# Kernel optimization log

Hardware: AMD Instinct MI355X
Metric: run time of the kernel (lower is better)

## Reference

```python
import jax, jax.numpy as jnp
import numpy as np

B, C, Q, D = 64, 2, 64, 4096
VOCAB = 30000


def setup_inputs() -> dict:
    key = jax.random.key(0)
    k1, k2, k3, k4, k5 = jax.random.split(key, 5)
    simmat = jax.random.uniform(k1, (B, C, Q, D), dtype=jnp.float32, minval=-1.0, maxval=1.0)
    dlens = jax.random.randint(k2, (B,), D // 2, D + 1, dtype=jnp.int32)
    qlens = jax.random.randint(k3, (B,), Q // 2, Q + 1, dtype=jnp.int32)
    dtoks = jax.random.randint(k4, (B, D), 0, VOCAB, dtype=jnp.int32)
    qtoks = jax.random.randint(k5, (B, Q), 0, VOCAB, dtype=jnp.int32)
    # -1 marks padding tokens beyond the true lengths
    dtoks = jnp.where(jnp.arange(D)[None, :] < dlens[:, None], dtoks, -1)
    qtoks = jnp.where(jnp.arange(Q)[None, :] < qlens[:, None], qtoks, -1)
    return {"simmat": simmat, "dlens": dlens, "dtoks": dtoks, "qtoks": qtoks, "nbins": 29}


def reference(simmat, dlens, dtoks, qtoks, nbins):
    b, c, q, d = simmat.shape
    # bin index per similarity value (int truncation, as in torch .int())
    bins = ((simmat + 1.00001) / 2.0 * (nbins - 1)).astype(jnp.int32)  # [B,C,Q,D]
    # weight = 1 where both doc token and query token are real (not padding)
    w = ((dtoks != -1)[:, None, :] & (qtoks != -1)[:, :, None]).astype(simmat.dtype)  # [B,Q,D]
    wb = jnp.broadcast_to(w[:, None, :, :], (b, c, q, d))
    # vectorized weighted histogram: scatter-add along bins per (b,c,q) row
    rows = jnp.arange(b * c * q)[:, None]
    hist = jnp.zeros((b * c * q, nbins), dtype=simmat.dtype)
    hist = hist.at[rows, bins.reshape(-1, d)].add(wb.reshape(-1, d))
    return hist.reshape(b, c, q, nbins)
```

## Files before the change

### kernel.cpp

```cpp
#include <hip/hip_runtime.h>

#define THREADS 256
#define NGROUP  16
#define HSTRIDE 33


template <int CHUNKS>
__global__ __launch_bounds__(THREADS) void count_hist_kernel(
    const float* __restrict__ simmat,
    const int*   __restrict__ dlens,
    const int*   __restrict__ qtoks,
    float*       __restrict__ out,
    int C, int Q, int D, int nbins)
{
    const int row = blockIdx.x;
    const int q   = row % Q;
    const int b   = row / (C * Q);
    const int tid = threadIdx.x;

    __shared__ unsigned int hist[NGROUP * HSTRIDE];
    unsigned int* __restrict__ gh = &hist[(tid >> 4) * HSTRIDE];

    const int  dlen   = dlens[b];
    const bool qvalid = (qtoks[b * Q + q] != -1);

    float4 s[CHUNKS];
    int    idx[CHUNKS];
    if (qvalid) {
        const float* __restrict__ srow = simmat + (size_t)row * D;
        #pragma unroll
        for (int c = 0; c < CHUNKS; ++c) {
            idx[c] = tid * 4 + c * (THREADS * 4);
            const int a = (idx[c] < dlen) ? idx[c] : 0;
            s[c] = *(const float4*)(srow + a);
        }
    }

    for (int i = tid; i < NGROUP * HSTRIDE; i += THREADS) hist[i] = 0u;
    __syncthreads();

    if (qvalid) {
        const float scale = 0.5f * (float)(nbins - 1);
        #pragma unroll
        for (int c = 0; c < CHUNKS; ++c) {
            const int bx = (int)((s[c].x + 1.00001f) * scale) & 31;
            const int by = (int)((s[c].y + 1.00001f) * scale) & 31;
            const int bz = (int)((s[c].z + 1.00001f) * scale) & 31;
            const int bw = (int)((s[c].w + 1.00001f) * scale) & 31;
            const int base = idx[c];
            if (base + 0 < dlen) atomicAdd(&gh[bx], 1u);
            if (base + 1 < dlen) atomicAdd(&gh[by], 1u);
            if (base + 2 < dlen) atomicAdd(&gh[bz], 1u);
            if (base + 3 < dlen) atomicAdd(&gh[bw], 1u);
        }
    }
    __syncthreads();

    if (tid < nbins) {
        unsigned int v = 0;
        #pragma unroll
        for (int g = 0; g < NGROUP; ++g) v += hist[g * HSTRIDE + tid];
        out[(size_t)row * nbins + tid] = (float)v;
    }
}

__global__ __launch_bounds__(THREADS) void count_hist_generic(
    const float* __restrict__ simmat,
    const int*   __restrict__ dlens,
    const int*   __restrict__ qtoks,
    float*       __restrict__ out,
    int C, int Q, int D, int nbins)
{
    const int row = blockIdx.x;
    const int q   = row % Q;
    const int b   = row / (C * Q);
    const int tid = threadIdx.x;

    __shared__ unsigned int hist[NGROUP * HSTRIDE];
    unsigned int* __restrict__ gh = &hist[(tid >> 4) * HSTRIDE];

    for (int i = tid; i < NGROUP * HSTRIDE; i += THREADS) hist[i] = 0u;
    __syncthreads();

    const int  dlen   = dlens[b];
    const bool qvalid = (qtoks[b * Q + q] != -1);

    if (qvalid) {
        const float* __restrict__ srow = simmat + (size_t)row * D;
        const float scale = 0.5f * (float)(nbins - 1);
        for (int i = tid; i < dlen; i += THREADS) {
            const float sv = srow[i];
            const int bn = (int)((sv + 1.00001f) * scale) & 31;
            atomicAdd(&gh[bn], 1u);
        }
    }
    __syncthreads();

    if (tid < nbins) {
        unsigned int v = 0;
        #pragma unroll
        for (int g = 0; g < NGROUP; ++g) v += hist[g * HSTRIDE + tid];
        out[(size_t)row * nbins + tid] = (float)v;
    }
}

extern "C" void kernel_launch(void* const* d_in, const int* in_sizes, int n_in,
                              void* d_out, int out_size, void* d_ws, size_t ws_size,
                              hipStream_t stream) {
    const float* simmat = (const float*)d_in[0];
    const int*   dlens  = (const int*)d_in[1];
    const int*   qtoks  = (const int*)d_in[3];

    const int B = in_sizes[1];
    const int D = in_sizes[2] / B;
    const int Q = in_sizes[3] / B;
    const int C = in_sizes[0] / (B * Q * D);
    const int nbins = out_size / (B * C * Q);

    float* out = (float*)d_out;
    const int rows = B * C * Q;

    if (D == THREADS * 4 * 4) {
        count_hist_kernel<4><<<rows, THREADS, 0, stream>>>(
            simmat, dlens, qtoks, out, C, Q, D, nbins);
    } else {
        count_hist_generic<<<rows, THREADS, 0, stream>>>(
            simmat, dlens, qtoks, out, C, Q, D, nbins);
    }
}
```

Baseline: 18.98 us.

## Map one histogram row per wavefront with double-buffered loads

```diff
diff --git a/kernel.cpp b/kernel.cpp
--- a/kernel.cpp
+++ b/kernel.cpp
@@ -1,66 +1,98 @@
 #include <hip/hip_runtime.h>
 
 #define THREADS 256
-#define NGROUP  16
+#define WAVES   4
+#define GPW     4
 #define HSTRIDE 33
 
 
-template <int CHUNKS>
-__global__ __launch_bounds__(THREADS) void count_hist_kernel(
+template <int STEPS>
+__global__ __launch_bounds__(THREADS) void count_hist_wave(
     const float* __restrict__ simmat,
     const int*   __restrict__ dlens,
     const int*   __restrict__ qtoks,
     float*       __restrict__ out,
-    int C, int Q, int D, int nbins)
+    int C, int Q, int D, int nbins, int nrows)
 {
-    const int row = blockIdx.x;
-    const int q   = row % Q;
-    const int b   = row / (C * Q);
-    const int tid = threadIdx.x;
+    const int tid  = threadIdx.x;
+    const int wave = tid >> 6;
+    const int lane = tid & 63;
+    const int row  = blockIdx.x * WAVES + wave;
 
-    __shared__ unsigned int hist[NGROUP * HSTRIDE];
-    unsigned int* __restrict__ gh = &hist[(tid >> 4) * HSTRIDE];
+    __shared__ unsigned int hist[WAVES * GPW * HSTRIDE];
+
+    if (row >= nrows) return;
+    const int q = row % Q;
+    const int b = row / (C * Q);
+
+    unsigned int* __restrict__ wh = &hist[wave * GPW * HSTRIDE];
+    unsigned int* __restrict__ gh = &wh[(lane >> 4) * HSTRIDE];
+
+    #pragma unroll
+    for (int i = lane; i < GPW * HSTRIDE; i += 64) wh[i] = 0u;
 
     const int  dlen   = dlens[b];
     const bool qvalid = (qtoks[b * Q + q] != -1);
 
-    float4 s[CHUNKS];
-    int    idx[CHUNKS];
     if (qvalid) {
         const float* __restrict__ srow = simmat + (size_t)row * D;
-        #pragma unroll
-        for (int c = 0; c < CHUNKS; ++c) {
-            idx[c] = tid * 4 + c * (THREADS * 4);
-            const int a = (idx[c] < dlen) ? idx[c] : 0;
-            s[c] = *(const float4*)(srow + a);
-        }
+        const float scale = 0.5f * (float)(nbins - 1);
+        const int e0 = lane * 4;
+
+        float4 A[4], Bv[4];
+
+        auto LOADB = [&](float4* buf, int t0) {
+            #pragma unroll
+            for (int s = 0; s < 4; ++s) {
+                const int stepBase = (t0 + s) * 256;
+                if (stepBase < dlen) {
+                    const int e = stepBase + e0;
+                    const int a = (e < dlen) ? e : 0;
+                    buf[s] = *(const float4*)(srow + a);
+                }
+            }
+        };
+        auto PROC = [&](const float4* buf, int t0) {
+            #pragma unroll
+            for (int s = 0; s < 4; ++s) {
+                const int stepBase = (t0 + s) * 256;
+                if (stepBase >= dlen) continue;
+                const float4 v = buf[s];
+                const int e  = stepBase + e0;
+                const int bx = (int)((v.x + 1.00001f) * scale) & 31;
+                const int by = (int)((v.y + 1.00001f) * scale) & 31;
+                const int bz = (int)((v.z + 1.00001f) * scale) & 31;
+                const int bw = (int)((v.w + 1.00001f) * scale) & 31;
+                if (stepBase + 256 <= dlen) {
+                    atomicAdd(&gh[bx], 1u);
+                    atomicAdd(&gh[by], 1u);
+                    atomicAdd(&gh[bz], 1u);
+                    atomicAdd(&gh[bw], 1u);
+                } else {
+                    if (e + 0 < dlen) atomicAdd(&gh[bx], 1u);
+                    if (e + 1 < dlen) atomicAdd(&gh[by], 1u);
+                    if (e + 2 < dlen) atomicAdd(&gh[bz], 1u);
+                    if (e + 3 < dlen) atomicAdd(&gh[bw], 1u);
+                }
+            }
+        };
+
+        static_assert(STEPS == 16, "pipeline is written for 16 steps");
+        LOADB(A,  0);
+        LOADB(Bv, 4);
+        PROC (A,  0);
+        LOADB(A,  8);
+        PROC (Bv, 4);
+        LOADB(Bv, 12);
+        PROC (A,  8);
+        PROC (Bv, 12);
     }
 
-    for (int i = tid; i < NGROUP * HSTRIDE; i += THREADS) hist[i] = 0u;
-    __syncthreads();
-
-    if (qvalid) {
-        const float scale = 0.5f * (float)(nbins - 1);
-        #pragma unroll
-        for (int c = 0; c < CHUNKS; ++c) {
-            const int bx = (int)((s[c].x + 1.00001f) * scale) & 31;
-            const int by = (int)((s[c].y + 1.00001f) * scale) & 31;
-            const int bz = (int)((s[c].z + 1.00001f) * scale) & 31;
-            const int bw = (int)((s[c].w + 1.00001f) * scale) & 31;
-            const int base = idx[c];
-            if (base + 0 < dlen) atomicAdd(&gh[bx], 1u);
-            if (base + 1 < dlen) atomicAdd(&gh[by], 1u);
-            if (base + 2 < dlen) atomicAdd(&gh[bz], 1u);
-            if (base + 3 < dlen) atomicAdd(&gh[bw], 1u);
-        }
-    }
-    __syncthreads();
-
-    if (tid < nbins) {
+    if (lane < nbins) {
         unsigned int v = 0;
         #pragma unroll
-        for (int g = 0; g < NGROUP; ++g) v += hist[g * HSTRIDE + tid];
-        out[(size_t)row * nbins + tid] = (float)v;
+        for (int g = 0; g < GPW; ++g) v += wh[g * HSTRIDE + lane];
+        out[(size_t)row * nbins + lane] = (float)v;
     }
 }
 
@@ -76,10 +108,10 @@
     const int b   = row / (C * Q);
     const int tid = threadIdx.x;
 
-    __shared__ unsigned int hist[NGROUP * HSTRIDE];
+    __shared__ unsigned int hist[16 * HSTRIDE];
     unsigned int* __restrict__ gh = &hist[(tid >> 4) * HSTRIDE];
 
-    for (int i = tid; i < NGROUP * HSTRIDE; i += THREADS) hist[i] = 0u;
+    for (int i = tid; i < 16 * HSTRIDE; i += THREADS) hist[i] = 0u;
     __syncthreads();
 
     const int  dlen   = dlens[b];
@@ -99,7 +131,7 @@
     if (tid < nbins) {
         unsigned int v = 0;
         #pragma unroll
-        for (int g = 0; g < NGROUP; ++g) v += hist[g * HSTRIDE + tid];
+        for (int g = 0; g < 16; ++g) v += hist[g * HSTRIDE + tid];
         out[(size_t)row * nbins + tid] = (float)v;
     }
 }
@@ -120,9 +152,10 @@
     float* out = (float*)d_out;
     const int rows = B * C * Q;
 
-    if (D == THREADS * 4 * 4) {
-        count_hist_kernel<4><<<rows, THREADS, 0, stream>>>(
-            simmat, dlens, qtoks, out, C, Q, D, nbins);
+    if (D == 16 * 256) {
+        const int grid = (rows + WAVES - 1) / WAVES;
+        count_hist_wave<16><<<grid, THREADS, 0, stream>>>(
+            simmat, dlens, qtoks, out, C, Q, D, nbins, rows);
     } else {
         count_hist_generic<<<rows, THREADS, 0, stream>>>(
             simmat, dlens, qtoks, out, C, Q, D, nbins);
```

New measurement: 25.22 us. 32.9% more time.

## Use per-wave histogram slices to drop a block barrier and early-exit padded rows

Applied to the files above, without the earlier changes.

```diff
diff --git a/kernel.cpp b/kernel.cpp
--- a/kernel.cpp
+++ b/kernel.cpp
@@ -1,6 +1,7 @@
 #include <hip/hip_runtime.h>
 
 #define THREADS 256
+#define GPW     4
 #define NGROUP  16
 #define HSTRIDE 33
 
@@ -13,54 +14,72 @@
     float*       __restrict__ out,
     int C, int Q, int D, int nbins)
 {
-    const int row = blockIdx.x;
-    const int q   = row % Q;
-    const int b   = row / (C * Q);
-    const int tid = threadIdx.x;
+    const int row  = blockIdx.x;
+    const int tid  = threadIdx.x;
+    const int wave = tid >> 6;
+    const int lane = tid & 63;
+    const int q    = row % Q;
+    const int b    = row / (C * Q);
 
     __shared__ unsigned int hist[NGROUP * HSTRIDE];
-    unsigned int* __restrict__ gh = &hist[(tid >> 4) * HSTRIDE];
 
-    const int  dlen   = dlens[b];
     const bool qvalid = (qtoks[b * Q + q] != -1);
+    if (!qvalid) {
+        if (tid < nbins) out[(size_t)row * nbins + tid] = 0.0f;
+        return;
+    }
+    const int dlen = dlens[b];
 
-    float4 s[CHUNKS];
+    const float* __restrict__ srow = simmat + (size_t)row * D;
+    float4 v[CHUNKS];
     int    idx[CHUNKS];
-    if (qvalid) {
-        const float* __restrict__ srow = simmat + (size_t)row * D;
-        #pragma unroll
-        for (int c = 0; c < CHUNKS; ++c) {
-            idx[c] = tid * 4 + c * (THREADS * 4);
-            const int a = (idx[c] < dlen) ? idx[c] : 0;
-            s[c] = *(const float4*)(srow + a);
+    #pragma unroll
+    for (int c = 0; c < CHUNKS; ++c) {
+        idx[c] = tid * 4 + c * (THREADS * 4);
+        const int a = (2 * idx[c] < D) ? idx[c]
+                                       : ((idx[c] < dlen) ? idx[c] : 0);
+        v[c] = *(const float4*)(srow + a);
+    }
+
+    unsigned int* __restrict__ wh = &hist[wave * GPW * HSTRIDE];
+    #pragma unroll
+    for (int i = lane; i < GPW * HSTRIDE; i += 64) wh[i] = 0u;
+
+    unsigned int* __restrict__ gh = &wh[(lane >> 4) * HSTRIDE];
+    const float scale = 0.5f * (float)(nbins - 1);
+    const float bias  = 1.00001f * scale;
+
+    #pragma unroll
+    for (int c = 0; c < CHUNKS; ++c) {
+        const int stepBase = c * (THREADS * 4);
+        if (stepBase >= dlen) continue;
+        const float4 f = v[c];
+        const int bx = (int)fmaf(f.x, scale, bias) & 31;
+        const int by = (int)fmaf(f.y, scale, bias) & 31;
+        const int bz = (int)fmaf(f.z, scale, bias) & 31;
+        const int bw = (int)fmaf(f.w, scale, bias) & 31;
+        const bool full = (stepBase + THREADS * 4 <= dlen);
+        if (full) {
+            atomicAdd(&gh[bx], 1u);
+            atomicAdd(&gh[by], 1u);
+            atomicAdd(&gh[bz], 1u);
+            atomicAdd(&gh[bw], 1u);
+        } else {
+            const int e = idx[c];
+            if (e + 0 < dlen) atomicAdd(&gh[bx], 1u);
+            if (e + 1 < dlen) atomicAdd(&gh[by], 1u);
+            if (e + 2 < dlen) atomicAdd(&gh[bz], 1u);
+            if (e + 3 < dlen) atomicAdd(&gh[bw], 1u);
         }
     }
 
-    for (int i = tid; i < NGROUP * HSTRIDE; i += THREADS) hist[i] = 0u;
-    __syncthreads();
-
-    if (qvalid) {
-        const float scale = 0.5f * (float)(nbins - 1);
-        #pragma unroll
-        for (int c = 0; c < CHUNKS; ++c) {
-            const int bx = (int)((s[c].x + 1.00001f) * scale) & 31;
-            const int by = (int)((s[c].y + 1.00001f) * scale) & 31;
-            const int bz = (int)((s[c].z + 1.00001f) * scale) & 31;
-            const int bw = (int)((s[c].w + 1.00001f) * scale) & 31;
-            const int base = idx[c];
-            if (base + 0 < dlen) atomicAdd(&gh[bx], 1u);
-            if (base + 1 < dlen) atomicAdd(&gh[by], 1u);
-            if (base + 2 < dlen) atomicAdd(&gh[bz], 1u);
-            if (base + 3 < dlen) atomicAdd(&gh[bw], 1u);
-        }
-    }
     __syncthreads();
 
     if (tid < nbins) {
-        unsigned int v = 0;
+        unsigned int t = 0;
         #pragma unroll
-        for (int g = 0; g < NGROUP; ++g) v += hist[g * HSTRIDE + tid];
-        out[(size_t)row * nbins + tid] = (float)v;
+        for (int g = 0; g < NGROUP; ++g) t += hist[g * HSTRIDE + tid];
+        out[(size_t)row * nbins + tid] = (float)t;
     }
 }
 
@@ -97,10 +116,10 @@
     __syncthreads();
 
     if (tid < nbins) {
-        unsigned int v = 0;
+        unsigned int t = 0;
         #pragma unroll
-        for (int g = 0; g < NGROUP; ++g) v += hist[g * HSTRIDE + tid];
-        out[(size_t)row * nbins + tid] = (float)v;
+        for (int g = 0; g < NGROUP; ++g) t += hist[g * HSTRIDE + tid];
+        out[(size_t)row * nbins + tid] = (float)t;
     }
 }
 
@@ -120,7 +139,7 @@
     float* out = (float*)d_out;
     const int rows = B * C * Q;
 
-    if (D == THREADS * 4 * 4) {
+    if (D == THREADS * 4 * 4 && nbins <= 32) {
         count_hist_kernel<4><<<rows, THREADS, 0, stream>>>(
             simmat, dlens, qtoks, out, C, Q, D, nbins);
     } else {
```

Result: no change. 19.03 us (+0.3%).
